# Kernel optimization log

Measured on AMD Instinct MI355X. Metric: run time of the kernel, lower is better.

Reference implementation:

```python
import jax, jax.numpy as jnp
import numpy as np

B, S, E, H = 4, 1024, 1024, 16
D = E // H          # head_dim = 64
F = 4 * E           # mlp inner = 4096
EPS = 1e-5


def _layernorm(x, scale, bias):
    mu = jnp.mean(x, axis=-1, keepdims=True)
    var = jnp.var(x, axis=-1, keepdims=True)
    return (x - mu) * jax.lax.rsqrt(var + EPS) * scale + bias


def setup_inputs() -> dict:
    key = jax.random.key(0)
    ks = jax.random.split(key, 8)
    std = 0.02
    return {
        "hidden_states": jax.random.normal(ks[0], (B, S, E), jnp.float32),
        "ln1_scale": jnp.ones((E,), jnp.float32),
        "ln1_bias": jnp.zeros((E,), jnp.float32),
        # Conv1D kernels stored as (out_features, in_features), applied as x @ k.T
        "w_attn": jax.random.normal(ks[1], (3 * E, E), jnp.float32) * std,
        "b_attn": jnp.zeros((3 * E,), jnp.float32),
        "w_proj": jax.random.normal(ks[2], (E, E), jnp.float32) * std,
        "b_proj": jnp.zeros((E,), jnp.float32),
        "ln2_scale": jnp.ones((E,), jnp.float32),
        "ln2_bias": jnp.zeros((E,), jnp.float32),
        "w_fc": jax.random.normal(ks[3], (F, E), jnp.float32) * std,
        "b_fc": jnp.zeros((F,), jnp.float32),
        "w_proj2": jax.random.normal(ks[4], (E, F), jnp.float32) * std,
        "b_proj2": jnp.zeros((E,), jnp.float32),
    }


def reference(hidden_states, ln1_scale, ln1_bias, w_attn, b_attn, w_proj, b_proj,
              ln2_scale, ln2_bias, w_fc, b_fc, w_proj2, b_proj2):
    x = hidden_states
    # --- attention sub-block ---
    h = _layernorm(x, ln1_scale, ln1_bias)
    qkv = h @ w_attn.T + b_attn                      # [B,S,3E]
    q, k, v = jnp.split(qkv, 3, axis=2)
    q = q.reshape(B, S, H, D) / jnp.sqrt(jnp.float32(D))
    k = k.reshape(B, S, H, D)
    v = v.reshape(B, S, H, D)
    # NOTE: source sets attention_bias = None, so NO causal mask is applied.
    logits = jnp.einsum("bqhd,bkhd->bhqk", q, k)     # [B,H,S,S]
    attn = jax.nn.softmax(logits, axis=-1)
    o = jnp.einsum("bhqk,bkhd->bqhd", attn, v).reshape(B, S, E)
    o = o @ w_proj.T + b_proj
    x = x + o
    # --- mlp sub-block ---
    h = _layernorm(x, ln2_scale, ln2_bias)
    m = jax.nn.gelu(h @ w_fc.T + b_fc, approximate=True)  # gelu_new
    m = m @ w_proj2.T + b_proj2
    return x + m
```

## Files before the change

### kernel.cpp

```cpp
#include <hip/hip_runtime.h>

#define DEV __device__ __forceinline__

using bf16x8 = __attribute__((ext_vector_type(8))) __bf16;
using f32x4  = __attribute__((ext_vector_type(4))) float;
typedef unsigned int u32;
typedef unsigned short u16;
typedef unsigned long long u64;

static constexpr int Bb = 4, Ss = 1024, Ee = 1024, Hh = 16, Dd = 64, Ff = 4096;
static constexpr int Mm = Bb * Ss;

DEV u16 f2bf(float f) {
  union { float f; u32 u; } v; v.f = f;
  u32 r = v.u + 0x7fffu + ((v.u >> 16) & 1u);
  return (u16)(r >> 16);
}

DEV void gload16(const void* g, void* lds) {
  __builtin_amdgcn_global_load_lds(
      (const __attribute__((address_space(1))) void*)(u64)g,
      (__attribute__((address_space(3))) void*)(u32)(u64)lds,
      16, 0, 0);
}

DEV float gelu_tanh(float x) {
  float x3 = x * x * x;
  float t  = tanhf(0.7978845608028654f * (x + 0.044715f * x3));
  return 0.5f * x * (1.0f + t);
}

DEV int swz(int row, int col) { return row * 64 + (col ^ ((row & 7) << 3)); }

__global__ __launch_bounds__(256) void cvt_bf16(const float* __restrict__ in,
                                                u16* __restrict__ out, int n) {
  int i = (blockIdx.x * 256 + threadIdx.x) * 8;
  if (i >= n) return;
  float4 a = *(const float4*)(in + i);
  float4 b = *(const float4*)(in + i + 4);
  uint4 o;
  o.x = (u32)f2bf(a.x) | ((u32)f2bf(a.y) << 16);
  o.y = (u32)f2bf(a.z) | ((u32)f2bf(a.w) << 16);
  o.z = (u32)f2bf(b.x) | ((u32)f2bf(b.y) << 16);
  o.w = (u32)f2bf(b.z) | ((u32)f2bf(b.w) << 16);
  *(uint4*)(out + i) = o;
}

__global__ __launch_bounds__(256) void ln_kernel(const float* __restrict__ x,
                                                 const float* __restrict__ scale,
                                                 const float* __restrict__ bias,
                                                 u16* __restrict__ h) {
  const int row = blockIdx.x, tid = threadIdx.x;
  const float4 v = ((const float4*)(x + (size_t)row * Ee))[tid];
  float s  = v.x + v.y + v.z + v.w;
  float ss = v.x * v.x + v.y * v.y + v.z * v.z + v.w * v.w;
  for (int m = 1; m < 64; m <<= 1) {
    s  += __shfl_xor(s, m, 64);
    ss += __shfl_xor(ss, m, 64);
  }
  __shared__ float red[8];
  const int w = tid >> 6, ln = tid & 63;
  if (ln == 0) { red[w * 2] = s; red[w * 2 + 1] = ss; }
  __syncthreads();
  s  = red[0] + red[2] + red[4] + red[6];
  ss = red[1] + red[3] + red[5] + red[7];
  const float mu   = s * (1.0f / Ee);
  const float var  = ss * (1.0f / Ee) - mu * mu;
  const float rstd = rsqrtf(var + 1e-5f);
  const float4 sc = ((const float4*)scale)[tid];
  const float4 bi = ((const float4*)bias)[tid];
  ushort4 o;
  o.x = f2bf((v.x - mu) * rstd * sc.x + bi.x);
  o.y = f2bf((v.y - mu) * rstd * sc.y + bi.y);
  o.z = f2bf((v.z - mu) * rstd * sc.z + bi.z);
  o.w = f2bf((v.w - mu) * rstd * sc.w + bi.w);
  ((ushort4*)(h + (size_t)row * Ee))[tid] = o;
}

template <int EPI>
__global__ __launch_bounds__(256) void gemm_bt(
    const u16* __restrict__ A, const u16* __restrict__ Bw,
    const float* __restrict__ bias, const float* __restrict__ resid,
    float* __restrict__ outf, u16* __restrict__ outb,
    u16* __restrict__ q, u16* __restrict__ k, u16* __restrict__ v,
    int N, int K) {
  __shared__ u16 As[128 * 32];
  __shared__ u16 Bs[128 * 32];
  const int tid = threadIdx.x;
  const int w = tid >> 6, ln = tid & 63;
  const int lr = ln & 15, lg = ln >> 4;
  const int tm = blockIdx.y * 128, tn = blockIdx.x * 128;
  const int wr = (w >> 1) * 64, wc = (w & 1) * 64;

  f32x4 zero4 = {0.f, 0.f, 0.f, 0.f};
  f32x4 acc[4][4];
#pragma unroll
  for (int i = 0; i < 4; ++i)
#pragma unroll
    for (int j = 0; j < 4; ++j) acc[i][j] = zero4;

  const int srow = tid >> 2;
  const int scol = (tid & 3) * 8;
  const u16* aP = A  + (size_t)(tm + srow) * K + scol;
  const u16* bP = Bw + (size_t)(tn + srow) * K + scol;
  const size_t rstep = (size_t)64 * K;
  u16* aL0 = &As[w * 512];
  u16* aL1 = &As[2048 + w * 512];
  u16* bL0 = &Bs[w * 512];
  u16* bL1 = &Bs[2048 + w * 512];

  for (int k0 = 0; k0 < K; k0 += 32) {
    gload16(aP + k0, aL0);
    gload16(aP + rstep + k0, aL1);
    gload16(bP + k0, bL0);
    gload16(bP + rstep + k0, bL1);
    __syncthreads();
    bf16x8 af[4], bfrag[4];
#pragma unroll
    for (int mi = 0; mi < 4; ++mi)
      af[mi] = *(const bf16x8*)&As[(wr + mi * 16 + lr) * 32 + lg * 8];
#pragma unroll
    for (int ni = 0; ni < 4; ++ni)
      bfrag[ni] = *(const bf16x8*)&Bs[(wc + ni * 16 + lr) * 32 + lg * 8];
#pragma unroll
    for (int mi = 0; mi < 4; ++mi)
#pragma unroll
      for (int ni = 0; ni < 4; ++ni)
        acc[mi][ni] = __builtin_amdgcn_mfma_f32_16x16x32_bf16(
            af[mi], bfrag[ni], acc[mi][ni], 0, 0, 0);
    __syncthreads();
  }

#pragma unroll
  for (int mi = 0; mi < 4; ++mi) {
#pragma unroll
    for (int ni = 0; ni < 4; ++ni) {
      const int gc = tn + wc + ni * 16 + lr;
#pragma unroll
      for (int j = 0; j < 4; ++j) {
        const int gr = tm + wr + mi * 16 + lg * 4 + j;
        float val = acc[mi][ni][j] + bias[gc];
        if constexpr (EPI == 0) {
          const int which = gc >> 10, hh = (gc >> 6) & 15, dd = gc & 63;
          const int bb = gr >> 10, ss2 = gr & 1023;
          const size_t dst = ((size_t)(bb * 16 + hh) * 1024 + ss2) * 64 + dd;
          if (which == 0)      q[dst] = f2bf(val * 0.125f);
          else if (which == 1) k[dst] = f2bf(val);
          else                 v[dst] = f2bf(val);
        } else if constexpr (EPI == 1) {
          const size_t idx = (size_t)gr * N + gc;
          outf[idx] = val + resid[idx];
        } else {
          outb[(size_t)gr * N + gc] = f2bf(gelu_tanh(val));
        }
      }
    }
  }
}

__global__ __launch_bounds__(256) void attn_kernel(const u16* __restrict__ qg,
                                                   const u16* __restrict__ kg,
                                                   const u16* __restrict__ vg,
                                                   u16* __restrict__ ao) {
  __shared__ u16 Qs[64 * 64], Ks[64 * 64], Vt[64 * 64], Ps[64 * 64];
  const int tid = threadIdx.x;
  const int w = tid >> 6, ln = tid & 63;
  const int lr = ln & 15, lg = ln >> 4;
  const int bh = blockIdx.y;
  const int q0 = blockIdx.x * 64;
  const size_t head = (size_t)bh * (Ss * Dd);

  {
    const u16* src = qg + head + (size_t)q0 * Dd;
#pragma unroll
    for (int i = 0; i < 2; ++i) {
      const int gi = i * 256 + tid, row = gi >> 3, g = gi & 7;
      *(uint4*)&Qs[row * 64 + ((g ^ (row & 7)) << 3)] = *(const uint4*)(src + gi * 8);
    }
  }

  f32x4 zero4 = {0.f, 0.f, 0.f, 0.f};
  f32x4 acc_o[4] = {zero4, zero4, zero4, zero4};
  float mrow[4] = {-1e30f, -1e30f, -1e30f, -1e30f};
  float lrow[4] = {0.f, 0.f, 0.f, 0.f};

  for (int kt = 0; kt < 16; ++kt) {
    __syncthreads();
    const u16* ksrc = kg + head + (size_t)kt * 64 * Dd;
    const u16* vsrc = vg + head + (size_t)kt * 64 * Dd;
#pragma unroll
    for (int i = 0; i < 2; ++i) {
      const int gi = i * 256 + tid, row = gi >> 3, g = gi & 7;
      *(uint4*)&Ks[row * 64 + ((g ^ (row & 7)) << 3)] = *(const uint4*)(ksrc + gi * 8);
    }
#pragma unroll
    for (int i = 0; i < 2; ++i) {
      const int kv = i * 32 + (tid >> 3), d0 = (tid & 7) * 8;
      uint4 dv = *(const uint4*)(vsrc + (size_t)kv * Dd + d0);
      const u16* pv = (const u16*)&dv;
#pragma unroll
      for (int j = 0; j < 8; ++j) {
        const int dd = d0 + j;
        Vt[dd * 64 + (((kv >> 3) ^ (dd & 7)) << 3) + (kv & 7)] = pv[j];
      }
    }
    __syncthreads();

    bf16x8 aq[2];
#pragma unroll
    for (int kk = 0; kk < 2; ++kk)
      aq[kk] = *(const bf16x8*)&Qs[swz(w * 16 + lr, kk * 32 + lg * 8)];
    f32x4 sa[4];
#pragma unroll
    for (int kf = 0; kf < 4; ++kf) {
      f32x4 s = zero4;
#pragma unroll
      for (int kk = 0; kk < 2; ++kk) {
        bf16x8 bk = *(const bf16x8*)&Ks[swz(kf * 16 + lr, kk * 32 + lg * 8)];
        s = __builtin_amdgcn_mfma_f32_16x16x32_bf16(aq[kk], bk, s, 0, 0, 0);
      }
      sa[kf] = s;
    }

#pragma unroll
    for (int j = 0; j < 4; ++j) {
      float mx = fmaxf(fmaxf(sa[0][j], sa[1][j]), fmaxf(sa[2][j], sa[3][j]));
      mx = fmaxf(mx, __shfl_xor(mx, 1, 64));
      mx = fmaxf(mx, __shfl_xor(mx, 2, 64));
      mx = fmaxf(mx, __shfl_xor(mx, 4, 64));
      mx = fmaxf(mx, __shfl_xor(mx, 8, 64));
      const float nm = fmaxf(mrow[j], mx);
      const float corr = __expf(mrow[j] - nm);
      mrow[j] = nm;
      float ssum = 0.f;
#pragma unroll
      for (int kf = 0; kf < 4; ++kf) {
        const float p = __expf(sa[kf][j] - nm);
        sa[kf][j] = p;
        ssum += p;
      }
      ssum += __shfl_xor(ssum, 1, 64);
      ssum += __shfl_xor(ssum, 2, 64);
      ssum += __shfl_xor(ssum, 4, 64);
      ssum += __shfl_xor(ssum, 8, 64);
      lrow[j] = lrow[j] * corr + ssum;
#pragma unroll
      for (int df = 0; df < 4; ++df) acc_o[df][j] *= corr;
    }

#pragma unroll
    for (int kf = 0; kf < 4; ++kf)
#pragma unroll
      for (int j = 0; j < 4; ++j)
        Ps[swz(w * 16 + lg * 4 + j, kf * 16 + lr)] = f2bf(sa[kf][j]);

    __syncthreads();

    bf16x8 ap[2];
#pragma unroll
    for (int kk = 0; kk < 2; ++kk)
      ap[kk] = *(const bf16x8*)&Ps[swz(w * 16 + lr, kk * 32 + lg * 8)];
#pragma unroll
    for (int df = 0; df < 4; ++df) {
#pragma unroll
      for (int kk = 0; kk < 2; ++kk) {
        bf16x8 bv = *(const bf16x8*)&Vt[swz(df * 16 + lr, kk * 32 + lg * 8)];
        acc_o[df] = __builtin_amdgcn_mfma_f32_16x16x32_bf16(ap[kk], bv, acc_o[df], 0, 0, 0);
      }
    }
  }

  const int b = bh >> 4, h = bh & 15;
#pragma unroll
  for (int df = 0; df < 4; ++df) {
#pragma unroll
    for (int j = 0; j < 4; ++j) {
      const int srow = q0 + w * 16 + lg * 4 + j;
      const int e = h * 64 + df * 16 + lr;
      ao[((size_t)b * Ss + srow) * Ee + e] = f2bf(acc_o[df][j] / lrow[j]);
    }
  }
}

extern "C" void kernel_launch(void* const* d_in, const int* in_sizes, int n_in,
                              void* d_out, int out_size, void* d_ws, size_t ws_size,
                              hipStream_t stream) {
  const float* x      = (const float*)d_in[0];
  const float* ln1_s  = (const float*)d_in[1];
  const float* ln1_b  = (const float*)d_in[2];
  const float* w_attn = (const float*)d_in[3];
  const float* b_attn = (const float*)d_in[4];
  const float* w_proj = (const float*)d_in[5];
  const float* b_proj = (const float*)d_in[6];
  const float* ln2_s  = (const float*)d_in[7];
  const float* ln2_b  = (const float*)d_in[8];
  const float* w_fc   = (const float*)d_in[9];
  const float* b_fc   = (const float*)d_in[10];
  const float* w_proj2= (const float*)d_in[11];
  const float* b_proj2= (const float*)d_in[12];
  float* out = (float*)d_out;

  char* base = (char*)d_ws;
  size_t off = 0;
  auto alloc = [&](size_t bytes) { char* p = base + off; off += bytes; return p; };
  u16* wA   = (u16*)alloc((size_t)3 * Ee * Ee * 2);
  u16* wP   = (u16*)alloc((size_t)Ee * Ee * 2);
  u16* wF   = (u16*)alloc((size_t)Ff * Ee * 2);
  u16* wP2  = (u16*)alloc((size_t)Ee * Ff * 2);
  u16* h1   = (u16*)alloc((size_t)Mm * Ee * 2);
  u16* qws  = (u16*)alloc((size_t)Mm * Ee * 2);
  u16* kws  = (u16*)alloc((size_t)Mm * Ee * 2);
  u16* vws  = (u16*)alloc((size_t)Mm * Ee * 2);
  u16* aws  = (u16*)alloc((size_t)Mm * Ee * 2);
  float* x1 = (float*)alloc((size_t)Mm * Ee * 4);
  u16* mfc  = qws;

  cvt_bf16<<<3 * Ee * Ee / 2048, 256, 0, stream>>>(w_attn, wA, 3 * Ee * Ee);
  cvt_bf16<<<Ee * Ee / 2048, 256, 0, stream>>>(w_proj, wP, Ee * Ee);
  cvt_bf16<<<Ff * Ee / 2048, 256, 0, stream>>>(w_fc, wF, Ff * Ee);
  cvt_bf16<<<Ee * Ff / 2048, 256, 0, stream>>>(w_proj2, wP2, Ee * Ff);

  ln_kernel<<<Mm, 256, 0, stream>>>(x, ln1_s, ln1_b, h1);
  gemm_bt<0><<<dim3(24, 32), 256, 0, stream>>>(h1, wA, b_attn, nullptr,
                                               nullptr, nullptr, qws, kws, vws,
                                               3 * Ee, Ee);
  attn_kernel<<<dim3(16, 64), 256, 0, stream>>>(qws, kws, vws, aws);
  gemm_bt<1><<<dim3(8, 32), 256, 0, stream>>>(aws, wP, b_proj, x,
                                              x1, nullptr, nullptr, nullptr, nullptr,
                                              Ee, Ee);
  ln_kernel<<<Mm, 256, 0, stream>>>(x1, ln2_s, ln2_b, h1);
  gemm_bt<2><<<dim3(32, 32), 256, 0, stream>>>(h1, wF, b_fc, nullptr,
                                               nullptr, mfc, nullptr, nullptr, nullptr,
                                               Ff, Ee);
  gemm_bt<1><<<dim3(8, 32), 256, 0, stream>>>(mfc, wP2, b_proj2, x1,
                                              out, nullptr, nullptr, nullptr, nullptr,
                                              Ee, Ff);
}
```

Baseline: 343.0 us.

## Triple-buffer GEMM LDS loads with swizzle, XCD block remap and fewer barriers

Rewrites the bf16 GEMM main loop to prefetch two K-tiles ahead into a 3-stage LDS ring, using counted vmcnt waits and a single barrier per iteration in place of two __syncthreads. The LDS column chunk is XOR-swizzled by row to reduce bank conflicts on fragment reads. Block IDs are remapped across the 8 XCDs, and MFMA priority is raised with s_setprio. The change triples LDS use per block and adds a launch-bounds occupancy hint; the manual waitcnt accounting is fragile if the compiler reorders loads.

```diff
diff --git a/kernel.cpp b/kernel.cpp
--- a/kernel.cpp
+++ b/kernel.cpp
@@ -78,18 +78,23 @@
 }
 
 template <int EPI>
-__global__ __launch_bounds__(256) void gemm_bt(
+__global__ __launch_bounds__(256, 3) void gemm2(
     const u16* __restrict__ A, const u16* __restrict__ Bw,
     const float* __restrict__ bias, const float* __restrict__ resid,
     float* __restrict__ outf, u16* __restrict__ outb,
     u16* __restrict__ q, u16* __restrict__ k, u16* __restrict__ v,
     int N, int K) {
-  __shared__ u16 As[128 * 32];
-  __shared__ u16 Bs[128 * 32];
+  __shared__ u16 As[3][128 * 32];
+  __shared__ u16 Bs[3][128 * 32];
   const int tid = threadIdx.x;
   const int w = tid >> 6, ln = tid & 63;
   const int lr = ln & 15, lg = ln >> 4;
-  const int tm = blockIdx.y * 128, tn = blockIdx.x * 128;
+
+  const int nwg = gridDim.x * gridDim.y;
+  const int bid = blockIdx.y * gridDim.x + blockIdx.x;
+  const int sid = (bid & 7) * (nwg >> 3) + (bid >> 3);
+  const int bx = sid % gridDim.x, by = sid / gridDim.x;
+  const int tm = by * 128, tn = bx * 128;
   const int wr = (w >> 1) * 64, wc = (w & 1) * 64;
 
   f32x4 zero4 = {0.f, 0.f, 0.f, 0.f};
@@ -99,36 +104,56 @@
 #pragma unroll
     for (int j = 0; j < 4; ++j) acc[i][j] = zero4;
 
-  const int srow = tid >> 2;
-  const int scol = (tid & 3) * 8;
-  const u16* aP = A  + (size_t)(tm + srow) * K + scol;
-  const u16* bP = Bw + (size_t)(tn + srow) * K + scol;
-  const size_t rstep = (size_t)64 * K;
-  u16* aL0 = &As[w * 512];
-  u16* aL1 = &As[2048 + w * 512];
-  u16* bL0 = &Bs[w * 512];
-  u16* bL1 = &Bs[2048 + w * 512];
-
-  for (int k0 = 0; k0 < K; k0 += 32) {
-    gload16(aP + k0, aL0);
-    gload16(aP + rstep + k0, aL1);
-    gload16(bP + k0, bL0);
-    gload16(bP + rstep + k0, bL1);
-    __syncthreads();
-    bf16x8 af[4], bfrag[4];
-#pragma unroll
-    for (int mi = 0; mi < 4; ++mi)
-      af[mi] = *(const bf16x8*)&As[(wr + mi * 16 + lr) * 32 + lg * 8];
-#pragma unroll
-    for (int ni = 0; ni < 4; ++ni)
-      bfrag[ni] = *(const bf16x8*)&Bs[(wc + ni * 16 + lr) * 32 + lg * 8];
+  const int r0 = tid >> 2, sl = tid & 3;
+  const int cs = (sl ^ (r0 & 3)) * 8;
+  const u16* aP0 = A  + (size_t)(tm + r0) * K + cs;
+  const u16* aP1 = A  + (size_t)(tm + 64 + r0) * K + cs;
+  const u16* bP0 = Bw + (size_t)(tn + r0) * K + cs;
+  const u16* bP1 = Bw + (size_t)(tn + 64 + r0) * K + cs;
+
+  auto STAGE = [&](int buf, int k0) {
+    gload16(aP0 + k0, &As[buf][tid * 8]);
+    gload16(aP1 + k0, &As[buf][(256 + tid) * 8]);
+    gload16(bP0 + k0, &Bs[buf][tid * 8]);
+    gload16(bP1 + k0, &Bs[buf][(256 + tid) * 8]);
+  };
+
+  const int nt = K >> 5;
+  STAGE(0, 0);
+  STAGE(1, 32);
+  asm volatile("s_waitcnt vmcnt(4)" ::: "memory");
+  __builtin_amdgcn_s_barrier();
+  __builtin_amdgcn_sched_barrier(0);
+
+  for (int t = 0; t < nt; ++t) {
+    const int cur = t % 3;
+    const bool more = (t + 2) < nt;
+    if (more) STAGE((t + 2) % 3, (t + 2) << 5);
+
+    bf16x8 af[4], bb[4];
+#pragma unroll
+    for (int mi = 0; mi < 4; ++mi) {
+      const int row = wr + mi * 16 + lr;
+      af[mi] = *(const bf16x8*)&As[cur][row * 32 + ((lg ^ (row & 3)) << 3)];
+    }
+#pragma unroll
+    for (int ni = 0; ni < 4; ++ni) {
+      const int row = wc + ni * 16 + lr;
+      bb[ni] = *(const bf16x8*)&Bs[cur][row * 32 + ((lg ^ (row & 3)) << 3)];
+    }
+    __builtin_amdgcn_s_setprio(1);
 #pragma unroll
     for (int mi = 0; mi < 4; ++mi)
 #pragma unroll
       for (int ni = 0; ni < 4; ++ni)
         acc[mi][ni] = __builtin_amdgcn_mfma_f32_16x16x32_bf16(
-            af[mi], bfrag[ni], acc[mi][ni], 0, 0, 0);
-    __syncthreads();
+            af[mi], bb[ni], acc[mi][ni], 0, 0, 0);
+    __builtin_amdgcn_s_setprio(0);
+    __builtin_amdgcn_sched_barrier(0);
+    if (more) asm volatile("s_waitcnt vmcnt(4)" ::: "memory");
+    else      asm volatile("s_waitcnt vmcnt(0)" ::: "memory");
+    __builtin_amdgcn_s_barrier();
+    __builtin_amdgcn_sched_barrier(0);
   }
 
 #pragma unroll
@@ -142,8 +167,8 @@
         float val = acc[mi][ni][j] + bias[gc];
         if constexpr (EPI == 0) {
           const int which = gc >> 10, hh = (gc >> 6) & 15, dd = gc & 63;
-          const int bb = gr >> 10, ss2 = gr & 1023;
-          const size_t dst = ((size_t)(bb * 16 + hh) * 1024 + ss2) * 64 + dd;
+          const int bb2 = gr >> 10, ss2 = gr & 1023;
+          const size_t dst = ((size_t)(bb2 * 16 + hh) * 1024 + ss2) * 64 + dd;
           if (which == 0)      q[dst] = f2bf(val * 0.125f);
           else if (which == 1) k[dst] = f2bf(val);
           else                 v[dst] = f2bf(val);
@@ -321,18 +346,18 @@
   cvt_bf16<<<Ee * Ff / 2048, 256, 0, stream>>>(w_proj2, wP2, Ee * Ff);
 
   ln_kernel<<<Mm, 256, 0, stream>>>(x, ln1_s, ln1_b, h1);
-  gemm_bt<0><<<dim3(24, 32), 256, 0, stream>>>(h1, wA, b_attn, nullptr,
-                                               nullptr, nullptr, qws, kws, vws,
-                                               3 * Ee, Ee);
+  gemm2<0><<<dim3(24, 32), 256, 0, stream>>>(h1, wA, b_attn, nullptr,
+                                             nullptr, nullptr, qws, kws, vws,
+                                             3 * Ee, Ee);
   attn_kernel<<<dim3(16, 64), 256, 0, stream>>>(qws, kws, vws, aws);
-  gemm_bt<1><<<dim3(8, 32), 256, 0, stream>>>(aws, wP, b_proj, x,
-                                              x1, nullptr, nullptr, nullptr, nullptr,
-                                              Ee, Ee);
+  gemm2<1><<<dim3(8, 32), 256, 0, stream>>>(aws, wP, b_proj, x,
+                                            x1, nullptr, nullptr, nullptr, nullptr,
+                                            Ee, Ee);
   ln_kernel<<<Mm, 256, 0, stream>>>(x1, ln2_s, ln2_b, h1);
-  gemm_bt<2><<<dim3(32, 32), 256, 0, stream>>>(h1, wF, b_fc, nullptr,
-                                               nullptr, mfc, nullptr, nullptr, nullptr,
-                                               Ff, Ee);
-  gemm_bt<1><<<dim3(8, 32), 256, 0, stream>>>(mfc, wP2, b_proj2, x1,
-                                              out, nullptr, nullptr, nullptr, nullptr,
-                                              Ee, Ff);
-}
+  gemm2<2><<<dim3(32, 32), 256, 0, stream>>>(h1, wF, b_fc, nullptr,
+                                             nullptr, mfc, nullptr, nullptr, nullptr,
+                                             Ff, Ee);
+  gemm2<1><<<dim3(8, 32), 256, 0, stream>>>(mfc, wP2, b_proj2, x1,
+                                            out, nullptr, nullptr, nullptr, nullptr,
+                                            Ee, Ff);
+}
```

After: 285.3 us. 1.2x faster.
